# Kernel tuning notes

Measured on AMD Instinct MI355X. Metric: run time of the kernel, lower is better.

## Reference

```python
import jax, jax.numpy as jnp
import numpy as np

B, C, L = 128, 1, 4096


def setup_inputs() -> dict:
    key = jax.random.key(0)
    x_0 = jax.random.normal(key, (B, C, L), dtype=jnp.float32)
    return {"x_0": x_0}


def reference(x_0):
    # Original: per-sample F.conv1d(x, flip(x), padding=L-1).
    # Cross-correlation with a flipped kernel == full linear convolution:
    #   out[b, t] = sum_c sum_i x[b,c,i] * x[b,c,t-i],  t in [0, 2L-2]
    # Vectorized over batch and channels via vmap; summed over channels
    # (conv1d contracts input channels against the weight's channel dim).
    conv = jax.vmap(jax.vmap(lambda a: jnp.convolve(a, a, mode='full')))(x_0)  # [B, C, 2L-1]
    return conv.sum(axis=1)[:, None, :]  # [B, 1, 2L-1]
```

## Files before the change

kernel.cpp:

```cpp
#include <hip/hip_runtime.h>

#define LL    4096
#define OUTL  8191
#define FPAD  272
#define NPDW  2336
#define CB1   2352
#define RB    4704
#define BTOP  5887
#define NGUP  992
#define LDSDW 9824

typedef short v8s __attribute__((ext_vector_type(8)));
typedef float v4f __attribute__((ext_vector_type(4)));

__device__ __forceinline__ unsigned bf16b(float f) {
    unsigned u = __builtin_bit_cast(unsigned, f);
    u += 0x7fff + ((u >> 16) & 1);
    return u >> 16;
}
__device__ __forceinline__ unsigned pk(float lo, float hi) {
    return bf16b(lo) | (bf16b(hi) << 16);
}
__device__ __forceinline__ int swz(int g) { return g ^ (((g >> 3) & 3) << 1); }

struct Frag {
    unsigned x0, x1, x2, x3, y0, y1, y2, y3;
    uint4 b3, b2, b1, b0;
};

__global__ __launch_bounds__(512, 4)
void selfconv_mfma6(const float* __restrict__ xg, float* __restrict__ outg) {
    __shared__ unsigned lds[LDSDW];
    const int tid = threadIdx.x;
    const int blk = blockIdx.x;
    const int b   = blk & 127;
    const int id  = blk >> 7;
    const int rg  = (id == 0) ? 0 : (id == 1) ? 3 : (id == 2) ? 1 : 2;
    const int T0  = rg << 11;
    const float* __restrict__ xb = xg + b * LL;

#pragma unroll
    for (int rr = 0; rr < 2; ++rr) {
        int w = tid + rr * 512;
        if (w < 584) {
            int E = 8 * w - FPAD;
            float e0,e1,e2,e3,e4,e5,e6,e7,e8;
            if (E >= 0 && E + 8 < LL) {
                float4 fa = *(const float4*)(xb + E);
                float4 fb = *(const float4*)(xb + E + 4);
                e0=fa.x; e1=fa.y; e2=fa.z; e3=fa.w;
                e4=fb.x; e5=fb.y; e6=fb.z; e7=fb.w; e8=xb[E+8];
            } else {
                float t[9];
#pragma unroll
                for (int k = 0; k < 9; ++k) {
                    int e = E + k;
                    t[k] = (e >= 0 && e < LL) ? xb[e] : 0.f;
                }
                e0=t[0]; e1=t[1]; e2=t[2]; e3=t[3]; e4=t[4];
                e5=t[5]; e6=t[6]; e7=t[7]; e8=t[8];
            }
            uint4 d0{pk(e0,e1), pk(e2,e3), pk(e4,e5), pk(e6,e7)};
            uint4 d1{pk(e1,e2), pk(e3,e4), pk(e5,e6), pk(e7,e8)};
            *(uint4*)&lds[4 * w]       = d0;
            *(uint4*)&lds[CB1 + 4 * w] = d1;
        }
    }
    {
        int g = 224 + tid;
        int x0 = BTOP - 7 - 8 * g;
        float4 fa = *(const float4*)(xb + x0);
        float4 fb = *(const float4*)(xb + x0 + 4);
        uint4 o{pk(fb.w, fb.z), pk(fb.y, fb.x), pk(fa.w, fa.z), pk(fa.y, fa.x)};
        *(uint4*)&lds[RB + 4 * swz(g)] = o;
    }
    if (tid < 480) {
        int u = (tid < 224) ? tid : tid + 512;
        *(uint4*)&lds[RB + 4 * u] = uint4{0, 0, 0, 0};
    }
    __syncthreads();

    const int wv = tid >> 6, lane = tid & 63, ln16 = lane & 15, q = lane >> 4;

    int mn = 0x7fffffff, mx = -0x7fffffff;
#pragma unroll
    for (int u = 0; u < 2; ++u)
#pragma unroll
        for (int v = 0; v < 4; ++v) {
            int base = T0 + 256 * u + 512 * v;
            int iLo = base - (LL - 1); if (iLo < 0) iLo = 0;
            int iHi = base + 255;      if (iHi > LL - 1) iHi = LL - 1;
            int a = iLo - 256 * u; if (a < mn) mn = a;
            int c2 = iHi - 256 * u; if (c2 > mx) mx = c2;
        }
    const int base_   = mn - 15;
    const int i0start = base_ - ((base_ - 1) & 7);
    const int nch     = ((mx - i0start) >> 5) + 1;
    const int nw      = (nch - wv + 7) >> 3;
    const int i0w     = i0start + 32 * wv;

    const int s0p = i0w + ln16 + 8 * q + FPAD;
    const int aw  = (s0p >> 1) + ((s0p & 1) ? CB1 : 0);
    const int g3 = (4352 - T0 + i0w - 16 * ln16 + 8 * q) >> 3;
    const int bw = RB + 4 * swz(g3);

    v4f a00{0,0,0,0}, a01{0,0,0,0}, a02{0,0,0,0}, a03{0,0,0,0};
    v4f a10{0,0,0,0}, a11{0,0,0,0}, a12{0,0,0,0}, a13{0,0,0,0};

    auto ld = [&](Frag& F, int a, int w) {
        F.x0 = lds[a];       F.x1 = lds[a + 1];
        F.x2 = lds[a + 2];   F.x3 = lds[a + 3];
        F.y0 = lds[a + 128]; F.y1 = lds[a + 129];
        F.y2 = lds[a + 130]; F.y3 = lds[a + 131];
        F.b3 = *(const uint4*)&lds[w];
        F.b2 = *(const uint4*)&lds[w + 256];
        F.b1 = *(const uint4*)&lds[w + 512];
        F.b0 = *(const uint4*)&lds[w + 768];
    };
    auto mkA = [](unsigned u0, unsigned u1, unsigned u2, unsigned u3) {
        union { unsigned x[4]; v8s s; } z;
        z.x[0] = u0; z.x[1] = u1; z.x[2] = u2; z.x[3] = u3; return z.s;
    };
    auto mkB = [](uint4 v) {
        union { unsigned x[4]; v8s s; } z;
        z.x[0] = v.x; z.x[1] = v.y; z.x[2] = v.z; z.x[3] = v.w; return z.s;
    };
    auto cmp = [&](const Frag& F) {
        v8s A0 = mkA(F.x0, F.x1, F.x2, F.x3);
        v8s A1 = mkA(F.y0, F.y1, F.y2, F.y3);
        v8s B3 = mkB(F.b3), B2 = mkB(F.b2), B1 = mkB(F.b1), B0 = mkB(F.b0);
        a03 = __builtin_amdgcn_mfma_f32_16x16x32_bf16(A0, B3, a03, 0, 0, 0);
        a13 = __builtin_amdgcn_mfma_f32_16x16x32_bf16(A1, B3, a13, 0, 0, 0);
        a02 = __builtin_amdgcn_mfma_f32_16x16x32_bf16(A0, B2, a02, 0, 0, 0);
        a12 = __builtin_amdgcn_mfma_f32_16x16x32_bf16(A1, B2, a12, 0, 0, 0);
        a01 = __builtin_amdgcn_mfma_f32_16x16x32_bf16(A0, B1, a01, 0, 0, 0);
        a11 = __builtin_amdgcn_mfma_f32_16x16x32_bf16(A1, B1, a11, 0, 0, 0);
        a00 = __builtin_amdgcn_mfma_f32_16x16x32_bf16(A0, B0, a00, 0, 0, 0);
        a10 = __builtin_amdgcn_mfma_f32_16x16x32_bf16(A1, B0, a10, 0, 0, 0);
    };

    Frag F0, F1;
    int awE = aw, bwE = bw, awO = aw + 128, bwO = bw + 128;
    ld(F0, awE, bwE); awE += 256; bwE += 256;
    ld(F1, awO, bwO); awO += 256; bwO += 256;
    int c = 0;
    for (; c + 2 < nw; c += 2) {
        cmp(F0); ld(F0, awE, bwE); awE += 256; bwE += 256;
        cmp(F1); ld(F1, awO, bwO); awO += 256; bwO += 256;
    }
    cmp(F0);
    if (c + 1 < nw) cmp(F1);

    float* fs = (float*)lds;
    __syncthreads();
    if (wv >= 4) {
        int sb = (wv - 4) * 2304 + lane * 36;
        *(v4f*)&fs[sb]      = a00; *(v4f*)&fs[sb + 4]  = a10;
        *(v4f*)&fs[sb + 8]  = a01; *(v4f*)&fs[sb + 12] = a11;
        *(v4f*)&fs[sb + 16] = a02; *(v4f*)&fs[sb + 20] = a12;
        *(v4f*)&fs[sb + 24] = a03; *(v4f*)&fs[sb + 28] = a13;
    }
    __syncthreads();
    if (wv < 4) {
        int sb = wv * 2304 + lane * 36;
        a00 += *(const v4f*)&fs[sb];      a10 += *(const v4f*)&fs[sb + 4];
        a01 += *(const v4f*)&fs[sb + 8];  a11 += *(const v4f*)&fs[sb + 12];
        a02 += *(const v4f*)&fs[sb + 16]; a12 += *(const v4f*)&fs[sb + 20];
        a03 += *(const v4f*)&fs[sb + 24]; a13 += *(const v4f*)&fs[sb + 28];
    }
    __syncthreads();
    if (wv >= 1 && wv < 4) {
        int sb = (wv - 1) * 2304 + lane * 36;
        *(v4f*)&fs[sb]      = a00; *(v4f*)&fs[sb + 4]  = a10;
        *(v4f*)&fs[sb + 8]  = a01; *(v4f*)&fs[sb + 12] = a11;
        *(v4f*)&fs[sb + 16] = a02; *(v4f*)&fs[sb + 20] = a12;
        *(v4f*)&fs[sb + 24] = a03; *(v4f*)&fs[sb + 28] = a13;
    }
    __syncthreads();
    if (wv == 0) {
#pragma unroll
        for (int s = 0; s < 3; ++s) {
            int sb = s * 2304 + lane * 36;
            a00 += *(const v4f*)&fs[sb];      a10 += *(const v4f*)&fs[sb + 4];
            a01 += *(const v4f*)&fs[sb + 8];  a11 += *(const v4f*)&fs[sb + 12];
            a02 += *(const v4f*)&fs[sb + 16]; a12 += *(const v4f*)&fs[sb + 20];
            a03 += *(const v4f*)&fs[sb + 24]; a13 += *(const v4f*)&fs[sb + 28];
        }
        float* __restrict__ ob = outg + b * OUTL;
        const v4f* accs[8] = {&a00, &a10, &a01, &a11, &a02, &a12, &a03, &a13};
#pragma unroll
        for (int uv = 0; uv < 8; ++uv) {
            int u = uv & 1, v = uv >> 1;
            int tilebase = T0 + 256 * u + 512 * v;
            int tb = tilebase + 4 * q + 16 * ln16;
            v4f a = *accs[uv];
            if (tilebase + 255 < OUTL) {
                *(v4f*)&ob[tb] = a;
            } else {
#pragma unroll
                for (int r2 = 0; r2 < 4; ++r2)
                    if (tb + r2 < OUTL) ob[tb + r2] = a[r2];
            }
        }
    }
}

extern "C" void kernel_launch(void* const* d_in, const int* in_sizes, int n_in,
                              void* d_out, int out_size, void* d_ws, size_t ws_size,
                              hipStream_t stream) {
    const float* x = (const float*)d_in[0];
    float* out = (float*)d_out;
    selfconv_mfma6<<<dim3(512), dim3(512), 0, stream>>>(x, out);
}
```

Baseline: 61.39 us.

## Reuse LDS fragments across chunk steps with rotating register ring and full unroll

Result: no change. 61.29 us (-0.2%).

```diff
diff --git a/kernel.cpp b/kernel.cpp
--- a/kernel.cpp
+++ b/kernel.cpp
@@ -9,6 +9,7 @@
 #define BTOP  5887
 #define NGUP  992
 #define LDSDW 9824
+#define UNRL  17
 
 typedef short v8s __attribute__((ext_vector_type(8)));
 typedef float v4f __attribute__((ext_vector_type(4)));
@@ -23,13 +24,8 @@
 }
 __device__ __forceinline__ int swz(int g) { return g ^ (((g >> 3) & 3) << 1); }
 
-struct Frag {
-    unsigned x0, x1, x2, x3, y0, y1, y2, y3;
-    uint4 b3, b2, b1, b0;
-};
-
 __global__ __launch_bounds__(512, 4)
-void selfconv_mfma6(const float* __restrict__ xg, float* __restrict__ outg) {
+void selfconv_mfma7(const float* __restrict__ xg, float* __restrict__ outg) {
     __shared__ unsigned lds[LDSDW];
     const int tid = threadIdx.x;
     const int blk = blockIdx.x;
@@ -60,8 +56,12 @@
                 e0=t[0]; e1=t[1]; e2=t[2]; e3=t[3]; e4=t[4];
                 e5=t[5]; e6=t[6]; e7=t[7]; e8=t[8];
             }
-            uint4 d0{pk(e0,e1), pk(e2,e3), pk(e4,e5), pk(e6,e7)};
-            uint4 d1{pk(e1,e2), pk(e3,e4), pk(e5,e6), pk(e7,e8)};
+            unsigned p0 = pk(e0, e1), p1 = pk(e2, e3);
+            unsigned p2 = pk(e4, e5), p3 = pk(e6, e7);
+            unsigned b8 = bf16b(e8);
+            uint4 d0{p0, p1, p2, p3};
+            uint4 d1{(p0 >> 16) | (p1 << 16), (p1 >> 16) | (p2 << 16),
+                     (p2 >> 16) | (p3 << 16), (p3 >> 16) | (b8 << 16)};
             *(uint4*)&lds[4 * w]       = d0;
             *(uint4*)&lds[CB1 + 4 * w] = d1;
         }
@@ -107,49 +107,53 @@
     v4f a00{0,0,0,0}, a01{0,0,0,0}, a02{0,0,0,0}, a03{0,0,0,0};
     v4f a10{0,0,0,0}, a11{0,0,0,0}, a12{0,0,0,0}, a13{0,0,0,0};
 
-    auto ld = [&](Frag& F, int a, int w) {
-        F.x0 = lds[a];       F.x1 = lds[a + 1];
-        F.x2 = lds[a + 2];   F.x3 = lds[a + 3];
-        F.y0 = lds[a + 128]; F.y1 = lds[a + 129];
-        F.y2 = lds[a + 130]; F.y3 = lds[a + 131];
-        F.b3 = *(const uint4*)&lds[w];
-        F.b2 = *(const uint4*)&lds[w + 256];
-        F.b1 = *(const uint4*)&lds[w + 512];
-        F.b0 = *(const uint4*)&lds[w + 768];
-    };
-    auto mkA = [](unsigned u0, unsigned u1, unsigned u2, unsigned u3) {
+    auto mkA = [](const unsigned* p) {
         union { unsigned x[4]; v8s s; } z;
-        z.x[0] = u0; z.x[1] = u1; z.x[2] = u2; z.x[3] = u3; return z.s;
+        z.x[0] = p[0]; z.x[1] = p[1]; z.x[2] = p[2]; z.x[3] = p[3];
+        return z.s;
     };
     auto mkB = [](uint4 v) {
         union { unsigned x[4]; v8s s; } z;
         z.x[0] = v.x; z.x[1] = v.y; z.x[2] = v.z; z.x[3] = v.w; return z.s;
     };
-    auto cmp = [&](const Frag& F) {
-        v8s A0 = mkA(F.x0, F.x1, F.x2, F.x3);
-        v8s A1 = mkA(F.y0, F.y1, F.y2, F.y3);
-        v8s B3 = mkB(F.b3), B2 = mkB(F.b2), B1 = mkB(F.b1), B0 = mkB(F.b0);
-        a03 = __builtin_amdgcn_mfma_f32_16x16x32_bf16(A0, B3, a03, 0, 0, 0);
-        a13 = __builtin_amdgcn_mfma_f32_16x16x32_bf16(A1, B3, a13, 0, 0, 0);
-        a02 = __builtin_amdgcn_mfma_f32_16x16x32_bf16(A0, B2, a02, 0, 0, 0);
-        a12 = __builtin_amdgcn_mfma_f32_16x16x32_bf16(A1, B2, a12, 0, 0, 0);
-        a01 = __builtin_amdgcn_mfma_f32_16x16x32_bf16(A0, B1, a01, 0, 0, 0);
-        a11 = __builtin_amdgcn_mfma_f32_16x16x32_bf16(A1, B1, a11, 0, 0, 0);
-        a00 = __builtin_amdgcn_mfma_f32_16x16x32_bf16(A0, B0, a00, 0, 0, 0);
-        a10 = __builtin_amdgcn_mfma_f32_16x16x32_bf16(A1, B0, a10, 0, 0, 0);
-    };
-
-    Frag F0, F1;
-    int awE = aw, bwE = bw, awO = aw + 128, bwO = bw + 128;
-    ld(F0, awE, bwE); awE += 256; bwE += 256;
-    ld(F1, awO, bwO); awO += 256; bwO += 256;
-    int c = 0;
-    for (; c + 2 < nw; c += 2) {
-        cmp(F0); ld(F0, awE, bwE); awE += 256; bwE += 256;
-        cmp(F1); ld(F1, awO, bwO); awO += 256; bwO += 256;
-    }
-    cmp(F0);
-    if (c + 1 < nw) cmp(F1);
+
+    uint4 Hb[8];
+    unsigned Ab[3][4];
+#pragma unroll
+    for (int j = 0; j < 7; ++j) Hb[j] = *(const uint4*)&lds[bw + 128 * j];
+    Hb[7] = uint4{0, 0, 0, 0};
+#pragma unroll
+    for (int k = 0; k < 4; ++k) {
+        Ab[0][k] = lds[aw + k];
+        Ab[1][k] = lds[aw + 128 + k];
+        Ab[2][k] = 0u;
+    }
+
+#pragma unroll
+    for (int t = 0; t < UNRL; ++t) {
+        if (t < nw) {
+            if (t + 1 < nw) {
+                Hb[(t + 7) & 7] = *(const uint4*)&lds[bw + 128 * (t + 7)];
+                const int an = aw + 128 * (t + 2);
+#pragma unroll
+                for (int k = 0; k < 4; ++k) Ab[(t + 2) % 3][k] = lds[an + k];
+            }
+            v8s A0 = mkA(Ab[t % 3]);
+            v8s A1 = mkA(Ab[(t + 1) % 3]);
+            v8s B3 = mkB(Hb[t & 7]),       B2 = mkB(Hb[(t + 2) & 7]);
+            v8s B1 = mkB(Hb[(t + 4) & 7]), B0 = mkB(Hb[(t + 6) & 7]);
+            __builtin_amdgcn_s_setprio(1);
+            a03 = __builtin_amdgcn_mfma_f32_16x16x32_bf16(A0, B3, a03, 0, 0, 0);
+            a13 = __builtin_amdgcn_mfma_f32_16x16x32_bf16(A1, B3, a13, 0, 0, 0);
+            a02 = __builtin_amdgcn_mfma_f32_16x16x32_bf16(A0, B2, a02, 0, 0, 0);
+            a12 = __builtin_amdgcn_mfma_f32_16x16x32_bf16(A1, B2, a12, 0, 0, 0);
+            a01 = __builtin_amdgcn_mfma_f32_16x16x32_bf16(A0, B1, a01, 0, 0, 0);
+            a11 = __builtin_amdgcn_mfma_f32_16x16x32_bf16(A1, B1, a11, 0, 0, 0);
+            a00 = __builtin_amdgcn_mfma_f32_16x16x32_bf16(A0, B0, a00, 0, 0, 0);
+            a10 = __builtin_amdgcn_mfma_f32_16x16x32_bf16(A1, B0, a10, 0, 0, 0);
+            __builtin_amdgcn_s_setprio(0);
+        }
+    }
 
     float* fs = (float*)lds;
     __syncthreads();
@@ -210,5 +214,5 @@
                               hipStream_t stream) {
     const float* x = (const float*)d_in[0];
     float* out = (float*)d_out;
-    selfconv_mfma6<<<dim3(512), dim3(512), 0, stream>>>(x, out);
-}
+    selfconv_mfma7<<<dim3(512), dim3(512), 0, stream>>>(x, out);
+}
```
